# Kernel tuning notes

Hardware: AMD Instinct MI355X
Metric: run time of the kernel (lower is better)

Reference implementation:

```python
import jax, jax.numpy as jnp
import numpy as np

B, CIN, H, W = 32, 16, 64, 64
COUT, K, STRIDE = 32, 3, 1


def setup_inputs() -> dict:
    key = jax.random.key(0)
    k1, k2, k3 = jax.random.split(key, 3)
    x = jax.random.normal(k1, (B, CIN, H, W), dtype=jnp.float32)
    # per-location kernels (Ho, Wo, Cout, Cin, K, K); kaiming-ish scale
    fan_in = CIN * K * K
    bound = float(np.sqrt(3.0 / fan_in))
    weights = jax.random.uniform(k2, (H, W, COUT, CIN, K, K), dtype=jnp.float32,
                                 minval=-bound, maxval=bound)
    bias = jax.random.normal(k3, (H, W, COUT), dtype=jnp.float32)
    return {"x": x, "weights": weights, "bias": bias}


def reference(x, weights, bias):
    Ho, Wo, co, ci, k, _ = weights.shape
    pad = k // 2
    if k % 2 == 1:
        padding = [(pad, pad), (pad, pad)]
    else:
        padding = [(pad - 1, pad), (pad - 1, pad)]
    # im2col: (B, ci*k*k, Ho, Wo); feature dim ordered channel-slowest, matching
    # torch's (C, k, k) flatten after unfold+permute.
    patches = jax.lax.conv_general_dilated_patches(
        x, (k, k), (STRIDE, STRIDE), padding)
    w = weights.reshape(Ho, Wo, co, ci * k * k)
    # per-location matmul: out[b,o,h,w] = sum_p patches[b,p,h,w] * w[h,w,o,p]
    out = jnp.einsum('bphw,hwop->bohw', patches, w)
    out = out + bias.transpose(2, 0, 1)[None]  # (1, Cout, Ho, Wo)
    return out
```

## Files before the change

kernel.cpp:

```cpp
#include <hip/hip_runtime.h>


#define BB      32
#define CIN     16
#define HH      64
#define WW      64
#define COUT    32
#define PP      144
#define WT      8
#define NCOL    10
#define BSTRIDE 498
#define ZOFF    480

typedef float v4f __attribute__((ext_vector_type(4)));
typedef short v8s __attribute__((ext_vector_type(8)));

__device__ __forceinline__ unsigned short f2bf(float f) {
    unsigned int u = __builtin_bit_cast(unsigned int, f);
    u += 0x7fffu + ((u >> 16) & 1u);
    return (unsigned short)(u >> 16);
}
__device__ __forceinline__ unsigned int pk2(float a, float b) {
    return (unsigned int)f2bf(a) | ((unsigned int)f2bf(b) << 16);
}

union U16 { uint4 u; v8s s; };

__global__ __launch_bounds__(512, 4) void xonv_kernel(
    const float* __restrict__ x,
    const float* __restrict__ weights,
    const float* __restrict__ bias,
    float* __restrict__ out)
{
    const int t  = threadIdx.x;
    const int bi = blockIdx.x;

    const int xcd  = bi & 7;
    const int rest = bi >> 3;
    const int wg   = rest & 7;
    const int h    = (rest >> 3) * 8 + xcd;
    const int w0   = wg * WT;

    __shared__ alignas(16) unsigned char smraw[36864];
    unsigned short* xl = (unsigned short*)smraw;
    float*          ol = (float*)smraw;

    if (t < 256) {
        const int b = t >> 3, k = t & 7;
        ((unsigned int*)smraw)[b * 249 + 240 + k] = 0u;
    }

    const bool wg0    = (wg == 0);
    const int  wstart = wg0 ? 0 : (w0 - 4);
#pragma unroll
    for (int s = 0; s < 3; ++s) {
        const int seg = t + s * 512;
        const int b   = seg / 48;
        const int cr  = seg % 48;
        const int c   = cr / 3;
        const int r   = cr % 3;
        const int row = h + r - 1;
        const bool rvalid = ((unsigned)row < HH);

        float win[16];
        if (rvalid) {
            const float* src = x + ((size_t)(b * CIN + c)) * (HH * WW) + row * WW;
#pragma unroll
            for (int k = 0; k < 4; ++k) {
                const int col4 = wstart + 4 * k;
                float4 f = {0.f, 0.f, 0.f, 0.f};
                if (col4 <= WW - 4) f = *(const float4*)(src + col4);
                win[4 * k + 0] = f.x; win[4 * k + 1] = f.y;
                win[4 * k + 2] = f.z; win[4 * k + 3] = f.w;
            }
        } else {
#pragma unroll
            for (int k = 0; k < 16; ++k) win[k] = 0.f;
        }

        float vals[NCOL];
        if (wg0) {
            vals[0] = 0.f;
#pragma unroll
            for (int j = 1; j < NCOL; ++j) vals[j] = win[j - 1];
        } else {
#pragma unroll
            for (int j = 0; j < NCOL; ++j) vals[j] = win[j + 3];
        }

        unsigned int* d32 = (unsigned int*)(xl + b * BSTRIDE + cr * NCOL);
#pragma unroll
        for (int k = 0; k < 5; ++k)
            d32[k] = pk2(vals[2 * k], vals[2 * k + 1]);
    }
    __syncthreads();

    const int l  = t & 63;
    const int wv = t >> 6;
    const int lm = l & 15;
    const int q  = l >> 4;
    const int w  = w0 + wv;

    const float* wlocp = weights + (size_t)(h * WW + w) * (COUT * PP);
    const float* wl0   = wlocp + (size_t)lm * PP;
    const float* wl1   = wlocp + (size_t)(lm + 16) * PP;

    const unsigned short* xr0 = xl + lm * BSTRIDE;
    const unsigned short* xr1 = xl + (lm + 16) * BSTRIDE;

    v4f acc00 = {0,0,0,0}, acc01 = {0,0,0,0};
    v4f acc10 = {0,0,0,0}, acc11 = {0,0,0,0};

#pragma unroll
    for (int kc = 0; kc < 5; ++kc) {
        const int p0 = kc * 32 + q * 8;

        v8s a0, a1;
#pragma unroll
        for (int j = 0; j < 8; ++j) {
            const int pj  = p0 + j;
            const int c   = (pj * 57) >> 9;
            const int rem = pj - c * 9;
            const int rr  = (rem * 11) >> 5;
            const int kw  = rem - rr * 3;
            int hw = (c * 3 + rr) * NCOL + wv + kw;
            hw = (pj < PP) ? hw : (ZOFF + (pj - PP));
            a0[j] = (short)xr0[hw];
            a1[j] = (short)xr1[hw];
        }

        v8s b0 = {0,0,0,0,0,0,0,0};
        v8s b1 = {0,0,0,0,0,0,0,0};
        if (p0 < PP) {
            float4 f0 = *(const float4*)(wl0 + p0);
            float4 f1 = *(const float4*)(wl0 + p0 + 4);
            float4 g0 = *(const float4*)(wl1 + p0);
            float4 g1 = *(const float4*)(wl1 + p0 + 4);
            U16 ub, ug;
            ub.u.x = pk2(f0.x, f0.y); ub.u.y = pk2(f0.z, f0.w);
            ub.u.z = pk2(f1.x, f1.y); ub.u.w = pk2(f1.z, f1.w);
            ug.u.x = pk2(g0.x, g0.y); ug.u.y = pk2(g0.z, g0.w);
            ug.u.z = pk2(g1.x, g1.y); ug.u.w = pk2(g1.z, g1.w);
            b0 = ub.s; b1 = ug.s;
        }

        acc00 = __builtin_amdgcn_mfma_f32_16x16x32_bf16(a0, b0, acc00, 0, 0, 0);
        acc01 = __builtin_amdgcn_mfma_f32_16x16x32_bf16(a0, b1, acc01, 0, 0, 0);
        acc10 = __builtin_amdgcn_mfma_f32_16x16x32_bf16(a1, b0, acc10, 0, 0, 0);
        acc11 = __builtin_amdgcn_mfma_f32_16x16x32_bf16(a1, b1, acc11, 0, 0, 0);
    }

    const float bia0 = bias[(size_t)(h * WW + w) * COUT + lm];
    const float bia1 = bias[(size_t)(h * WW + w) * COUT + 16 + lm];

    __syncthreads();

#pragma unroll
    for (int mt = 0; mt < 2; ++mt) {
#pragma unroll
        for (int j = 0; j < 4; ++j) {
            const int b = mt * 16 + q * 4 + j;
            const v4f& r0 = mt ? acc10 : acc00;
            const v4f& r1 = mt ? acc11 : acc01;
            ol[(b * COUT + lm) * 9 + wv]        = r0[j] + bia0;
            ol[(b * COUT + 16 + lm) * 9 + wv]   = r1[j] + bia1;
        }
    }
    __syncthreads();

    {
        const int seg = t >> 3;
        const int wj  = t & 7;
        float* ob = out + (size_t)h * WW + w0 + wj;
#pragma unroll
        for (int i = 0; i < 16; ++i) {
            const int bo = i * 64 + seg;
            ob[(size_t)bo * (HH * WW)] = ol[bo * 9 + wj];
        }
    }
}

extern "C" void kernel_launch(void* const* d_in, const int* in_sizes, int n_in,
                              void* d_out, int out_size, void* d_ws, size_t ws_size,
                              hipStream_t stream) {
    const float* x       = (const float*)d_in[0];
    const float* weights = (const float*)d_in[1];
    const float* bias    = (const float*)d_in[2];
    float* out           = (float*)d_out;
    (void)in_sizes; (void)n_in; (void)out_size; (void)d_ws; (void)ws_size;

    dim3 grid(512);
    dim3 block(512);
    hipLaunchKernelGGL(xonv_kernel, grid, block, 0, stream, x, weights, bias, out);
}
```

Measured before the change: 130.5 us.

## Use 32x32x16 MFMA with simplified padded x tile and prefetched weights

```diff
diff --git a/kernel.cpp b/kernel.cpp
--- a/kernel.cpp
+++ b/kernel.cpp
@@ -1,19 +1,17 @@
 #include <hip/hip_runtime.h>
 
 
-#define BB      32
 #define CIN     16
 #define HH      64
 #define WW      64
 #define COUT    32
 #define PP      144
 #define WT      8
-#define NCOL    10
-#define BSTRIDE 498
-#define ZOFF    480
+#define RSTRIDE 770
 
-typedef float v4f __attribute__((ext_vector_type(4)));
-typedef short v8s __attribute__((ext_vector_type(8)));
+typedef float v4f  __attribute__((ext_vector_type(4)));
+typedef float v16f __attribute__((ext_vector_type(16)));
+typedef short v8s  __attribute__((ext_vector_type(8)));
 
 __device__ __forceinline__ unsigned short f2bf(float f) {
     unsigned int u = __builtin_bit_cast(unsigned int, f);
@@ -23,8 +21,6 @@
 __device__ __forceinline__ unsigned int pk2(float a, float b) {
     return (unsigned int)f2bf(a) | ((unsigned int)f2bf(b) << 16);
 }
-
-union U16 { uint4 u; v8s s; };
 
 __global__ __launch_bounds__(512, 4) void xonv_kernel(
     const float* __restrict__ x,
@@ -40,131 +36,93 @@
     const int wg   = rest & 7;
     const int h    = (rest >> 3) * 8 + xcd;
     const int w0   = wg * WT;
+    const int wstart = w0 - 4;
 
-    __shared__ alignas(16) unsigned char smraw[36864];
+    __shared__ alignas(16) unsigned char smraw[49280];
     unsigned short* xl = (unsigned short*)smraw;
     float*          ol = (float*)smraw;
 
-    if (t < 256) {
-        const int b = t >> 3, k = t & 7;
-        ((unsigned int*)smraw)[b * 249 + 240 + k] = 0u;
-    }
-
-    const bool wg0    = (wg == 0);
-    const int  wstart = wg0 ? 0 : (w0 - 4);
+    {
+        const int rid0 = t >> 2;
+        const int sub  = t & 3;
+        int b  = rid0 / 48;
+        int cr = rid0 % 48;
+        const int col4  = wstart + sub * 4;
+        const bool colok = (col4 >= 0) && (col4 <= WW - 4);
 #pragma unroll
-    for (int s = 0; s < 3; ++s) {
-        const int seg = t + s * 512;
-        const int b   = seg / 48;
-        const int cr  = seg % 48;
-        const int c   = cr / 3;
-        const int r   = cr % 3;
-        const int row = h + r - 1;
-        const bool rvalid = ((unsigned)row < HH);
-
-        float win[16];
-        if (rvalid) {
-            const float* src = x + ((size_t)(b * CIN + c)) * (HH * WW) + row * WW;
-#pragma unroll
-            for (int k = 0; k < 4; ++k) {
-                const int col4 = wstart + 4 * k;
-                float4 f = {0.f, 0.f, 0.f, 0.f};
-                if (col4 <= WW - 4) f = *(const float4*)(src + col4);
-                win[4 * k + 0] = f.x; win[4 * k + 1] = f.y;
-                win[4 * k + 2] = f.z; win[4 * k + 3] = f.w;
+        for (int pass = 0; pass < 12; ++pass) {
+            const int c   = cr / 3;
+            const int r   = cr - c * 3;
+            const int row = h + r - 1;
+            float4 f = {0.f, 0.f, 0.f, 0.f};
+            if (colok && (unsigned)row < HH) {
+                f = *(const float4*)(x + ((size_t)(b * CIN + c)) * (HH * WW)
+                                       + row * WW + col4);
             }
-        } else {
-#pragma unroll
-            for (int k = 0; k < 16; ++k) win[k] = 0.f;
+            unsigned int* d = (unsigned int*)(xl + b * RSTRIDE + cr * 16 + sub * 4);
+            d[0] = pk2(f.x, f.y);
+            d[1] = pk2(f.z, f.w);
+            b += 2; cr += 32; if (cr >= 48) { cr -= 48; ++b; }
         }
-
-        float vals[NCOL];
-        if (wg0) {
-            vals[0] = 0.f;
-#pragma unroll
-            for (int j = 1; j < NCOL; ++j) vals[j] = win[j - 1];
-        } else {
-#pragma unroll
-            for (int j = 0; j < NCOL; ++j) vals[j] = win[j + 3];
-        }
-
-        unsigned int* d32 = (unsigned int*)(xl + b * BSTRIDE + cr * NCOL);
-#pragma unroll
-        for (int k = 0; k < 5; ++k)
-            d32[k] = pk2(vals[2 * k], vals[2 * k + 1]);
     }
     __syncthreads();
 
     const int l  = t & 63;
     const int wv = t >> 6;
-    const int lm = l & 15;
-    const int q  = l >> 4;
     const int w  = w0 + wv;
+    const int o  = l & 31;
+    const int kh = l >> 5;
+    const int ph = kh * 8;
 
-    const float* wlocp = weights + (size_t)(h * WW + w) * (COUT * PP);
-    const float* wl0   = wlocp + (size_t)lm * PP;
-    const float* wl1   = wlocp + (size_t)(lm + 16) * PP;
+    const float* wp = weights + (size_t)(h * WW + w) * (COUT * PP)
+                              + (size_t)o * PP + ph;
+    const int xbase = (l & 31) * RSTRIDE + wv + 3;
 
-    const unsigned short* xr0 = xl + lm * BSTRIDE;
-    const unsigned short* xr1 = xl + (lm + 16) * BSTRIDE;
+    v16f acc;
+#pragma unroll
+    for (int i = 0; i < 16; ++i) acc[i] = 0.f;
 
-    v4f acc00 = {0,0,0,0}, acc01 = {0,0,0,0};
-    v4f acc10 = {0,0,0,0}, acc11 = {0,0,0,0};
+    int dq = ph >> 2;
+    int mq = ph >> 2;
+
+    v4f c0 = *(const v4f*)(wp);
+    v4f c1 = *(const v4f*)(wp + 4);
 
 #pragma unroll
-    for (int kc = 0; kc < 5; ++kc) {
-        const int p0 = kc * 32 + q * 8;
+    for (int kc = 0; kc < 9; ++kc) {
+        v4f n0, n1;
+        if (kc < 8) {
+            n0 = *(const v4f*)(wp + (kc + 1) * 16);
+            n1 = *(const v4f*)(wp + (kc + 1) * 16 + 4);
+        }
 
-        v8s a0, a1;
+        v8s a;
+        const int base = xbase + dq * 16 + mq;
 #pragma unroll
         for (int j = 0; j < 8; ++j) {
-            const int pj  = p0 + j;
-            const int c   = (pj * 57) >> 9;
-            const int rem = pj - c * 9;
-            const int rr  = (rem * 11) >> 5;
-            const int kw  = rem - rr * 3;
-            int hw = (c * 3 + rr) * NCOL + wv + kw;
-            hw = (pj < PP) ? hw : (ZOFF + (pj - PP));
-            a0[j] = (short)xr0[hw];
-            a1[j] = (short)xr1[hw];
+            const int e  = mq + j;
+            const int tt = (e * 11) >> 5;
+            a[j] = (short)xl[base + j + 13 * tt];
         }
 
-        v8s b0 = {0,0,0,0,0,0,0,0};
-        v8s b1 = {0,0,0,0,0,0,0,0};
-        if (p0 < PP) {
-            float4 f0 = *(const float4*)(wl0 + p0);
-            float4 f1 = *(const float4*)(wl0 + p0 + 4);
-            float4 g0 = *(const float4*)(wl1 + p0);
-            float4 g1 = *(const float4*)(wl1 + p0 + 4);
-            U16 ub, ug;
-            ub.u.x = pk2(f0.x, f0.y); ub.u.y = pk2(f0.z, f0.w);
-            ub.u.z = pk2(f1.x, f1.y); ub.u.w = pk2(f1.z, f1.w);
-            ug.u.x = pk2(g0.x, g0.y); ug.u.y = pk2(g0.z, g0.w);
-            ug.u.z = pk2(g1.x, g1.y); ug.u.w = pk2(g1.z, g1.w);
-            b0 = ub.s; b1 = ug.s;
-        }
+        union { unsigned int u[4]; v8s s; } ub;
+        ub.u[0] = pk2(c0.x, c0.y); ub.u[1] = pk2(c0.z, c0.w);
+        ub.u[2] = pk2(c1.x, c1.y); ub.u[3] = pk2(c1.z, c1.w);
 
-        acc00 = __builtin_amdgcn_mfma_f32_16x16x32_bf16(a0, b0, acc00, 0, 0, 0);
-        acc01 = __builtin_amdgcn_mfma_f32_16x16x32_bf16(a0, b1, acc01, 0, 0, 0);
-        acc10 = __builtin_amdgcn_mfma_f32_16x16x32_bf16(a1, b0, acc10, 0, 0, 0);
-        acc11 = __builtin_amdgcn_mfma_f32_16x16x32_bf16(a1, b1, acc11, 0, 0, 0);
+        acc = __builtin_amdgcn_mfma_f32_32x32x16_bf16(a, ub.s, acc, 0, 0, 0);
+
+        c0 = n0; c1 = n1;
+        mq += 1; dq += 5; if (mq == 3) { mq = 0; dq += 1; }
     }
 
-    const float bia0 = bias[(size_t)(h * WW + w) * COUT + lm];
-    const float bia1 = bias[(size_t)(h * WW + w) * COUT + 16 + lm];
+    const float bia = bias[(size_t)(h * WW + w) * COUT + o];
 
     __syncthreads();
 
 #pragma unroll
-    for (int mt = 0; mt < 2; ++mt) {
-#pragma unroll
-        for (int j = 0; j < 4; ++j) {
-            const int b = mt * 16 + q * 4 + j;
-            const v4f& r0 = mt ? acc10 : acc00;
-            const v4f& r1 = mt ? acc11 : acc01;
-            ol[(b * COUT + lm) * 9 + wv]        = r0[j] + bia0;
-            ol[(b * COUT + 16 + lm) * 9 + wv]   = r1[j] + bia1;
-        }
+    for (int r = 0; r < 16; ++r) {
+        const int brow = (r & 3) + 8 * (r >> 2) + 4 * kh;
+        ol[(brow * COUT + o) * 9 + wv] = acc[r] + bia;
     }
     __syncthreads();
 
```

Measured after the change: 129.2 us. No clear change (-1.0%).
